# Kernel tuning notes

Hardware: AMD Instinct MI355X
Metric: run time of the kernel (lower is better)

## Reference

```python
import jax, jax.numpy as jnp
import numpy as np

B, N, D_IN, D_OUT, MAX_POS = 256, 256, 768, 300, 256
NEG_INF = -9e15
LEAKY_SLOPE = 0.2


def setup_inputs() -> dict:
    key = jax.random.key(0)
    ks = jax.random.split(key, 6)
    h = jax.random.normal(ks[0], (B, N, D_IN), dtype=jnp.float32)
    adj = (jax.random.uniform(ks[1], (B, N, N)) > 0.9).astype(jnp.float32)
    adj = jnp.maximum(adj, jnp.eye(N, dtype=jnp.float32)[None])
    positions = jax.random.randint(ks[2], (B, N), 0, MAX_POS)
    W = jax.random.normal(ks[3], (D_IN, D_OUT), dtype=jnp.float32) * (1.0 / np.sqrt(D_IN))
    a_src = jax.random.normal(ks[4], (1, D_OUT), dtype=jnp.float32) * 0.05
    a_dst = jax.random.normal(ks[5], (1, D_OUT), dtype=jnp.float32) * 0.05
    pos_table = jax.random.normal(jax.random.fold_in(key, 7), (MAX_POS, D_OUT), dtype=jnp.float32)
    return {"h": h, "adj": adj, "positions": positions, "W": W,
            "a_src": a_src, "a_dst": a_dst, "pos_table": pos_table}


def reference(h, adj, positions, W, a_src, a_dst, pos_table):
    # Wh = W(h) + position embedding          [B, N, D_OUT]
    Wh = jnp.einsum('bni,io->bno', h, W) + pos_table[positions]
    # additive attention scores
    f_src = jnp.einsum('bno,o->bn', Wh, a_src[0])  # [B, N]
    f_dst = jnp.einsum('bno,o->bn', Wh, a_dst[0])  # [B, N]
    e = f_src[:, :, None] + f_dst[:, None, :]      # [B, N, N]
    e = jnp.where(e >= 0, e, LEAKY_SLOPE * e)      # LeakyReLU(0.2)
    # adjacency masking + softmax over last dim
    masked = jnp.where(adj > 0, e, NEG_INF)
    attention = jax.nn.softmax(masked, axis=-1)
    # (eval mode: edge dropout and dropout are identity)
    h_prime = jnp.einsum('bnm,bmo->bno', attention, Wh)
    return h_prime, attention
```

## Files before the change

kernel.cpp:

```cpp
#include <hip/hip_runtime.h>

#define B_    256
#define N_    256
#define DIN   768
#define DOUT  300
#define DOUTP 320
#define M_    (B_*N_)
#define HP_ELEMS (M_*DOUT)
#define NEG_INF -9.0e15f

typedef _Float16 f16;
typedef __attribute__((ext_vector_type(8))) _Float16 f16x8;
typedef __attribute__((ext_vector_type(4))) _Float16 f16x4;
typedef __attribute__((ext_vector_type(4))) float    f32x4;

__global__ __launch_bounds__(256) void prep_wt(const float* __restrict__ W,
                                               f16* __restrict__ WtT) {
    int idx = blockIdx.x * 256 + threadIdx.x;
    if (idx >= DIN * DOUTP) return;
    int k = idx / DOUTP, n = idx - k * DOUTP;
    float v = (n < DOUT) ? W[k * DOUT + n] : 0.0f;
    WtT[(((size_t)(k >> 5) * DOUTP + n) << 5) + (k & 31)] = (f16)v;
}

__global__ __launch_bounds__(256, 3) void gemm1(
    const float* __restrict__ h, const f16* __restrict__ WtT,
    const int* __restrict__ positions,
    const float* __restrict__ a_src, const float* __restrict__ a_dst,
    const float* __restrict__ pos_table,
    f16* __restrict__ WhT2, float* __restrict__ f_src, float* __restrict__ f_dst)
{
    __shared__ f16 Ah[64 * 384];
    __shared__ float pfs[64][4], pfd[64][4];

    const int tid  = threadIdx.x;
    const int wave = tid >> 6, lane = tid & 63;
    const int quad = lane >> 4, c = lane & 15;
    const int rowbase = blockIdx.x * 64;
    const int cx7 = c & 7;

    const int crow = tid >> 2, cl4 = tid & 3;
    const float* cbase = h + (size_t)(rowbase + crow) * DIN;

    int boffs[5];
#pragma unroll
    for (int i = 0; i < 5; ++i) {
        int n = (wave * 5 + i) * 16 + c;
        boffs[i] = (n << 5) + (quad << 3);
    }

    f32x4 acc[4][5];
#pragma unroll
    for (int rt = 0; rt < 4; ++rt)
#pragma unroll
        for (int i = 0; i < 5; ++i) acc[rt][i] = (f32x4){0.f, 0.f, 0.f, 0.f};

    f16x8 bs[2][5];

#define CONV(HALF) do {                                                        \
    _Pragma("unroll")                                                          \
    for (int j_ = 0; j_ < 12; ++j_) {                                          \
        int c8_ = j_ * 4 + cl4;                                                \
        const float4* s_ = (const float4*)(cbase + (HALF) * 384 + c8_ * 8);    \
        float4 v0 = s_[0], v1 = s_[1];                                         \
        int slot_ = c8_ ^ (crow & 7);                                          \
        *(f16x8*)&Ah[crow * 384 + slot_ * 8] =                                 \
            (f16x8){(f16)v0.x, (f16)v0.y, (f16)v0.z, (f16)v0.w,                \
                    (f16)v1.x, (f16)v1.y, (f16)v1.z, (f16)v1.w};               \
    } } while (0)

#define PREF(KT, S) do {                                                       \
    const f16* p_ = WtT + (size_t)(KT) * (DOUTP * 32);                         \
    _Pragma("unroll")                                                          \
    for (int i_ = 0; i_ < 5; ++i_)                                             \
        bs[S][i_] = *(const f16x8*)(p_ + boffs[i_]);                           \
    } while (0)

#define COMPUTE(KT12, S) do {                                                  \
    const int k4_ = (KT12) * 4 + quad;                                         \
    __builtin_amdgcn_s_setprio(1);                                             \
    _Pragma("unroll")                                                          \
    for (int rt_ = 0; rt_ < 4; ++rt_) {                                        \
        f16x8 af = *(const f16x8*)&Ah[(rt_ * 16 + c) * 384 + ((k4_ ^ cx7) << 3)]; \
        _Pragma("unroll")                                                      \
        for (int i_ = 0; i_ < 5; ++i_)                                         \
            acc[rt_][i_] = __builtin_amdgcn_mfma_f32_16x16x32_f16(             \
                af, bs[S][i_], acc[rt_][i_], 0, 0, 0);                         \
    }                                                                          \
    __builtin_amdgcn_s_setprio(0);                                             \
    } while (0)

    CONV(0);
    __syncthreads();
    PREF(0, 0);
#pragma unroll
    for (int kt2 = 0; kt2 < 12; ++kt2) {
        const int ktA = 2 * kt2, ktB = 2 * kt2 + 1;
        PREF(ktB, 1);
        COMPUTE(ktA % 12, 0);
        if (ktB + 1 < 24) PREF(ktB + 1, 0);
        COMPUTE(ktB % 12, 1);
        if (kt2 == 5) {
            __syncthreads();
            CONV(1);
            __syncthreads();
        }
    }
#undef COMPUTE
#undef PREF
#undef CONV

    const int bidx = rowbase >> 8;
    const int ktb0 = (rowbase & 255) >> 5;

    int posr[4][4];
#pragma unroll
    for (int rt = 0; rt < 4; ++rt)
#pragma unroll
        for (int r = 0; r < 4; ++r)
            posr[rt][r] = positions[rowbase + rt * 16 + quad * 4 + r];

    float fs[4][4], fd[4][4];
#pragma unroll
    for (int rt = 0; rt < 4; ++rt)
#pragma unroll
        for (int r = 0; r < 4; ++r) { fs[rt][r] = 0.f; fd[rt][r] = 0.f; }

#pragma unroll
    for (int i = 0; i < 5; ++i) {
        int col = (wave * 5 + i) * 16 + c;
        if (col < DOUT) {
            float as = a_src[col], ad = a_dst[col];
#pragma unroll
            for (int rt = 0; rt < 4; ++rt)
#pragma unroll
                for (int r = 0; r < 4; ++r) {
                    float v = acc[rt][i][r] + pos_table[posr[rt][r] * DOUT + col];
                    acc[rt][i][r] = v;
                    fs[rt][r] += v * as;
                    fd[rt][r] += v * ad;
                }
        } else {
#pragma unroll
            for (int rt = 0; rt < 4; ++rt)
#pragma unroll
                for (int r = 0; r < 4; ++r) acc[rt][i][r] = 0.0f;
        }
    }
#pragma unroll
    for (int off = 1; off < 16; off <<= 1) {
#pragma unroll
        for (int rt = 0; rt < 4; ++rt)
#pragma unroll
            for (int r = 0; r < 4; ++r) {
                fs[rt][r] += __shfl_xor(fs[rt][r], off, 16);
                fd[rt][r] += __shfl_xor(fd[rt][r], off, 16);
            }
    }
    if (c == 0) {
#pragma unroll
        for (int rt = 0; rt < 4; ++rt)
#pragma unroll
            for (int r = 0; r < 4; ++r) {
                int row = rt * 16 + quad * 4 + r;
                pfs[row][wave] = fs[rt][r];
                pfd[row][wave] = fd[rt][r];
            }
    }
#pragma unroll
    for (int i = 0; i < 5; ++i) {
        int col = (wave * 5 + i) * 16 + c;
#pragma unroll
        for (int rt = 0; rt < 4; ++rt) {
            f16x4 u = (f16x4){(f16)acc[rt][i][0], (f16)acc[rt][i][1],
                              (f16)acc[rt][i][2], (f16)acc[rt][i][3]};
            size_t off = (((size_t)(bidx * 8 + ktb0 + (rt >> 1)) * DOUTP + col) << 5)
                         + (rt & 1) * 16 + quad * 4;
            *(f16x4*)(WhT2 + off) = u;
        }
    }
    __syncthreads();
    if (tid < 64) {
        f_src[rowbase + tid] = pfs[tid][0] + pfs[tid][1] + pfs[tid][2] + pfs[tid][3];
        f_dst[rowbase + tid] = pfd[tid][0] + pfd[tid][1] + pfd[tid][2] + pfd[tid][3];
    }
}

__global__ __launch_bounds__(256, 3) void fused2(
    const float* __restrict__ adj, const float* __restrict__ f_src,
    const float* __restrict__ f_dst, const f16* __restrict__ WhT2,
    float* __restrict__ att, float* __restrict__ hp)
{
    __shared__ f16 Pl[64 * 256];

    const int tid  = threadIdx.x;
    const int wave = tid >> 6, lane = tid & 63;
    const int quad = lane >> 4, c = lane & 15;
    const int rowbase = blockIdx.x * 64;
    const int bidx = rowbase >> 8;
    const int cx7 = c & 7;

    int boffs[5];
#pragma unroll
    for (int i = 0; i < 5; ++i) {
        int n = (wave * 5 + i) * 16 + c;
        boffs[i] = (n << 5) + (quad << 3);
    }
    const f16* wbase = WhT2 + (size_t)bidx * 8 * (DOUTP * 32);

    f16x8 bs[2][5];
#define PREF2(KT, S) do {                                                      \
    const f16* p_ = wbase + (size_t)(KT) * (DOUTP * 32);                       \
    _Pragma("unroll")                                                          \
    for (int i_ = 0; i_ < 5; ++i_)                                             \
        bs[S][i_] = *(const f16x8*)(p_ + boffs[i_]);                           \
    } while (0)

    {
        float4 fd4 = *(const float4*)(f_dst + bidx * N_ + lane * 4);
        const float* arow = adj + (size_t)(rowbase + wave * 16) * N_ + lane * 4;
        float4 nx0 = *(const float4*)arow;
        float4 nx1 = *(const float4*)(arow + N_);
        for (int rr = 0; rr < 16; ++rr) {
            float4 a4 = nx0;
            nx0 = nx1;
            if (rr + 2 < 16) nx1 = *(const float4*)(arow + (size_t)(rr + 2) * N_);
            const int lrow = wave * 16 + rr;
            const int row  = rowbase + lrow;
            float fsv = f_src[row];

            float v, e0, e1, e2, e3;
            v = fsv + fd4.x; v = v >= 0.f ? v : 0.2f * v; e0 = a4.x > 0.f ? v : NEG_INF;
            v = fsv + fd4.y; v = v >= 0.f ? v : 0.2f * v; e1 = a4.y > 0.f ? v : NEG_INF;
            v = fsv + fd4.z; v = v >= 0.f ? v : 0.2f * v; e2 = a4.z > 0.f ? v : NEG_INF;
            v = fsv + fd4.w; v = v >= 0.f ? v : 0.2f * v; e3 = a4.w > 0.f ? v : NEG_INF;

            float mx = fmaxf(fmaxf(e0, e1), fmaxf(e2, e3));
#pragma unroll
            for (int off = 1; off < 64; off <<= 1) mx = fmaxf(mx, __shfl_xor(mx, off, 64));

            float p0 = __expf(e0 - mx), p1 = __expf(e1 - mx);
            float p2 = __expf(e2 - mx), p3 = __expf(e3 - mx);
            float s = p0 + p1 + p2 + p3;
#pragma unroll
            for (int off = 1; off < 64; off <<= 1) s += __shfl_xor(s, off, 64);

            float inv = 1.0f / s;
            *(float4*)(att + (size_t)row * N_ + lane * 4) =
                make_float4(p0 * inv, p1 * inv, p2 * inv, p3 * inv);
            int slot = (lane >> 1) ^ (lrow & 7);
            *(f16x4*)&Pl[lrow * 256 + slot * 8 + (lane & 1) * 4] =
                (f16x4){(f16)(p0 * inv), (f16)(p1 * inv), (f16)(p2 * inv), (f16)(p3 * inv)};
        }
    }
    PREF2(0, 0);
    __syncthreads();

    f32x4 acc[4][5];
#pragma unroll
    for (int rt = 0; rt < 4; ++rt)
#pragma unroll
        for (int i = 0; i < 5; ++i) acc[rt][i] = (f32x4){0.f, 0.f, 0.f, 0.f};

#define COMPUTE2(KT, S) do {                                                   \
    const int k4_ = (KT) * 4 + quad;                                           \
    __builtin_amdgcn_s_setprio(1);                                             \
    _Pragma("unroll")                                                          \
    for (int rt_ = 0; rt_ < 4; ++rt_) {                                        \
        f16x8 af = *(const f16x8*)&Pl[(rt_ * 16 + c) * 256 + ((k4_ ^ cx7) << 3)]; \
        _Pragma("unroll")                                                      \
        for (int i_ = 0; i_ < 5; ++i_)                                         \
            acc[rt_][i_] = __builtin_amdgcn_mfma_f32_16x16x32_f16(             \
                af, bs[S][i_], acc[rt_][i_], 0, 0, 0);                         \
    }                                                                          \
    __builtin_amdgcn_s_setprio(0);                                             \
    } while (0)

#pragma unroll
    for (int kt2 = 0; kt2 < 4; ++kt2) {
        const int ktA = 2 * kt2, ktB = 2 * kt2 + 1;
        PREF2(ktB, 1);
        COMPUTE2(ktA, 0);
        if (ktB + 1 < 8) PREF2(ktB + 1, 0);
        COMPUTE2(ktB, 1);
    }
#undef COMPUTE2
#undef PREF2

#pragma unroll
    for (int i = 0; i < 5; ++i) {
        int col = (wave * 5 + i) * 16 + c;
        if (col < DOUT) {
#pragma unroll
            for (int rt = 0; rt < 4; ++rt) {
                int row0 = rowbase + rt * 16 + quad * 4;
#pragma unroll
                for (int r = 0; r < 4; ++r)
                    hp[(size_t)(row0 + r) * DOUT + col] = acc[rt][i][r];
            }
        }
    }
}

extern "C" void kernel_launch(void* const* d_in, const int* in_sizes, int n_in,
                              void* d_out, int out_size, void* d_ws, size_t ws_size,
                              hipStream_t stream)
{
    const float* h         = (const float*)d_in[0];
    const float* adj       = (const float*)d_in[1];
    const int*   positions = (const int*)d_in[2];
    const float* W         = (const float*)d_in[3];
    const float* a_src     = (const float*)d_in[4];
    const float* a_dst     = (const float*)d_in[5];
    const float* pos_table = (const float*)d_in[6];

    float* hp  = (float*)d_out;
    float* att = hp + HP_ELEMS;

    f16*   WtT   = (f16*)d_ws;
    f16*   WhT2  = WtT + (size_t)DOUTP * DIN;
    float* f_src = (float*)(WhT2 + (size_t)B_ * DOUTP * N_);
    float* f_dst = f_src + M_;

    hipLaunchKernelGGL(prep_wt, dim3((DIN * DOUTP + 255) / 256), dim3(256), 0, stream, W, WtT);
    hipLaunchKernelGGL(gemm1,   dim3(M_ / 64), dim3(256), 0, stream,
                       h, WtT, positions, a_src, a_dst, pos_table, WhT2, f_src, f_dst);
    hipLaunchKernelGGL(fused2,  dim3(M_ / 64), dim3(256), 0, stream,
                       adj, f_src, f_dst, WhT2, att, hp);
}
```

Baseline: 473.1 us.

## Load GEMM A operand directly into registers and relayout WhT2 intermediate

Removes the LDS staging of the fp32 h tile in gemm1. Each lane now loads its own MFMA A fragments straight from global memory into registers, double-buffered, and converts them to f16 just before the MFMAs, which drops the barriers and shared-memory traffic. The WhT2 intermediate layout changes so the epilogue writes 4-element chunks contiguous along the column. fused2 is adjusted to read this layout with two f16x4 loads per fragment. The register double buffering raises register pressure, so launch bounds drop to 2 blocks per SM, and the global A loads are narrower and less coalesced than the old cooperative copy.

Result: slower. 486.5 us (+2.8%).

```diff
diff --git a/kernel.cpp b/kernel.cpp
--- a/kernel.cpp
+++ b/kernel.cpp
@@ -23,24 +23,24 @@
     WtT[(((size_t)(k >> 5) * DOUTP + n) << 5) + (k & 31)] = (f16)v;
 }
 
-__global__ __launch_bounds__(256, 3) void gemm1(
+__global__ __launch_bounds__(256, 2) void gemm1(
     const float* __restrict__ h, const f16* __restrict__ WtT,
     const int* __restrict__ positions,
     const float* __restrict__ a_src, const float* __restrict__ a_dst,
     const float* __restrict__ pos_table,
     f16* __restrict__ WhT2, float* __restrict__ f_src, float* __restrict__ f_dst)
 {
-    __shared__ f16 Ah[64 * 384];
     __shared__ float pfs[64][4], pfd[64][4];
 
     const int tid  = threadIdx.x;
     const int wave = tid >> 6, lane = tid & 63;
     const int quad = lane >> 4, c = lane & 15;
     const int rowbase = blockIdx.x * 64;
-    const int cx7 = c & 7;
-
-    const int crow = tid >> 2, cl4 = tid & 3;
-    const float* cbase = h + (size_t)(rowbase + crow) * DIN;
+
+    const float* ab0 = h + (size_t)(rowbase + c) * DIN + quad * 8;
+    const float* ab1 = ab0 + 16 * DIN;
+    const float* ab2 = ab0 + 32 * DIN;
+    const float* ab3 = ab0 + 48 * DIN;
 
     int boffs[5];
 #pragma unroll
@@ -55,60 +55,62 @@
 #pragma unroll
         for (int i = 0; i < 5; ++i) acc[rt][i] = (f32x4){0.f, 0.f, 0.f, 0.f};
 
-    f16x8 bs[2][5];
-
-#define CONV(HALF) do {                                                        \
-    _Pragma("unroll")                                                          \
-    for (int j_ = 0; j_ < 12; ++j_) {                                          \
-        int c8_ = j_ * 4 + cl4;                                                \
-        const float4* s_ = (const float4*)(cbase + (HALF) * 384 + c8_ * 8);    \
-        float4 v0 = s_[0], v1 = s_[1];                                         \
-        int slot_ = c8_ ^ (crow & 7);                                          \
-        *(f16x8*)&Ah[crow * 384 + slot_ * 8] =                                 \
-            (f16x8){(f16)v0.x, (f16)v0.y, (f16)v0.z, (f16)v0.w,                \
-                    (f16)v1.x, (f16)v1.y, (f16)v1.z, (f16)v1.w};               \
-    } } while (0)
-
-#define PREF(KT, S) do {                                                       \
+    float4 av[2][4][2];
+    f16x8  bs[2][5];
+    f16x8  af[4];
+
+#define LOADA(KT, S) do {                                                      \
+    av[S][0][0] = *(const float4*)(ab0 + (KT) * 32);                           \
+    av[S][0][1] = *(const float4*)(ab0 + (KT) * 32 + 4);                       \
+    av[S][1][0] = *(const float4*)(ab1 + (KT) * 32);                           \
+    av[S][1][1] = *(const float4*)(ab1 + (KT) * 32 + 4);                       \
+    av[S][2][0] = *(const float4*)(ab2 + (KT) * 32);                           \
+    av[S][2][1] = *(const float4*)(ab2 + (KT) * 32 + 4);                       \
+    av[S][3][0] = *(const float4*)(ab3 + (KT) * 32);                           \
+    av[S][3][1] = *(const float4*)(ab3 + (KT) * 32 + 4);                       \
+} while (0)
+
+#define LOADB(KT, S) do {                                                      \
     const f16* p_ = WtT + (size_t)(KT) * (DOUTP * 32);                         \
     _Pragma("unroll")                                                          \
     for (int i_ = 0; i_ < 5; ++i_)                                             \
         bs[S][i_] = *(const f16x8*)(p_ + boffs[i_]);                           \
-    } while (0)
-
-#define COMPUTE(KT12, S) do {                                                  \
-    const int k4_ = (KT12) * 4 + quad;                                         \
+} while (0)
+
+#define CVT(S) do {                                                            \
+    _Pragma("unroll")                                                          \
+    for (int rt_ = 0; rt_ < 4; ++rt_) {                                        \
+        float4 u0 = av[S][rt_][0], u1 = av[S][rt_][1];                         \
+        af[rt_] = (f16x8){(f16)u0.x, (f16)u0.y, (f16)u0.z, (f16)u0.w,          \
+                          (f16)u1.x, (f16)u1.y, (f16)u1.z, (f16)u1.w};         \
+    } } while (0)
+
+#define COMP(S) do {                                                           \
     __builtin_amdgcn_s_setprio(1);                                             \
     _Pragma("unroll")                                                          \
-    for (int rt_ = 0; rt_ < 4; ++rt_) {                                        \
-        f16x8 af = *(const f16x8*)&Ah[(rt_ * 16 + c) * 384 + ((k4_ ^ cx7) << 3)]; \
+    for (int rt_ = 0; rt_ < 4; ++rt_)                                          \
         _Pragma("unroll")                                                      \
         for (int i_ = 0; i_ < 5; ++i_)                                         \
             acc[rt_][i_] = __builtin_amdgcn_mfma_f32_16x16x32_f16(             \
-                af, bs[S][i_], acc[rt_][i_], 0, 0, 0);                         \
-    }                                                                          \
+                af[rt_], bs[S][i_], acc[rt_][i_], 0, 0, 0);                    \
     __builtin_amdgcn_s_setprio(0);                                             \
-    } while (0)
-
-    CONV(0);
-    __syncthreads();
-    PREF(0, 0);
-#pragma unroll
-    for (int kt2 = 0; kt2 < 12; ++kt2) {
-        const int ktA = 2 * kt2, ktB = 2 * kt2 + 1;
-        PREF(ktB, 1);
-        COMPUTE(ktA % 12, 0);
-        if (ktB + 1 < 24) PREF(ktB + 1, 0);
-        COMPUTE(ktB % 12, 1);
-        if (kt2 == 5) {
-            __syncthreads();
-            CONV(1);
-            __syncthreads();
-        }
-    }
-#undef COMPUTE
-#undef PREF
-#undef CONV
+} while (0)
+
+    LOADA(0, 0);
+    LOADB(0, 0);
+#pragma unroll
+    for (int kt = 0; kt < 24; ++kt) {
+        if (kt + 1 < 24) {
+            LOADA(kt + 1, (kt + 1) & 1);
+            LOADB(kt + 1, (kt + 1) & 1);
+        }
+        CVT(kt & 1);
+        COMP(kt & 1);
+    }
+#undef COMP
+#undef CVT
+#undef LOADB
+#undef LOADA
 
     const int bidx = rowbase >> 8;
     const int ktb0 = (rowbase & 255) >> 5;
@@ -174,8 +176,8 @@
         for (int rt = 0; rt < 4; ++rt) {
             f16x4 u = (f16x4){(f16)acc[rt][i][0], (f16)acc[rt][i][1],
                               (f16)acc[rt][i][2], (f16)acc[rt][i][3]};
-            size_t off = (((size_t)(bidx * 8 + ktb0 + (rt >> 1)) * DOUTP + col) << 5)
-                         + (rt & 1) * 16 + quad * 4;
+            size_t off = (((size_t)(bidx * 8 + ktb0 + (rt >> 1)) * 8
+                           + (rt & 1) * 4 + quad) * DOUTP + col) * 4;
             *(f16x4*)(WhT2 + off) = u;
         }
     }
@@ -200,21 +202,19 @@
     const int bidx = rowbase >> 8;
     const int cx7 = c & 7;
 
-    int boffs[5];
-#pragma unroll
-    for (int i = 0; i < 5; ++i) {
-        int n = (wave * 5 + i) * 16 + c;
-        boffs[i] = (n << 5) + (quad << 3);
-    }
     const f16* wbase = WhT2 + (size_t)bidx * 8 * (DOUTP * 32);
 
     f16x8 bs[2][5];
 #define PREF2(KT, S) do {                                                      \
     const f16* p_ = wbase + (size_t)(KT) * (DOUTP * 32);                       \
     _Pragma("unroll")                                                          \
-    for (int i_ = 0; i_ < 5; ++i_)                                             \
-        bs[S][i_] = *(const f16x8*)(p_ + boffs[i_]);                           \
-    } while (0)
+    for (int i_ = 0; i_ < 5; ++i_) {                                           \
+        int n_ = (wave * 5 + i_) * 16 + c;                                     \
+        f16x4 lo_ = *(const f16x4*)(p_ + (2 * quad) * (DOUTP * 4) + n_ * 4);   \
+        f16x4 hi_ = *(const f16x4*)(p_ + (2 * quad + 1) * (DOUTP * 4) + n_ * 4); \
+        bs[S][i_] = (f16x8){lo_[0], lo_[1], lo_[2], lo_[3],                    \
+                            hi_[0], hi_[1], hi_[2], hi_[3]};                   \
+    } } while (0)
 
     {
         float4 fd4 = *(const float4*)(f_dst + bidx * N_ + lane * 4);
```
